# Kernel tuning notes

Measured on AMD Instinct MI355X. Metric: run time of the kernel, lower is better.

Reference implementation:

```python
import jax, jax.numpy as jnp
import numpy as np

DEGREE = 3
N_BASIS = 16


def _clamped_knots(n_basis, degree):
    # Clamped uniform knot vector on [0, 1]: degree+1 repeated knots at each end.
    n_interior = n_basis - degree - 1
    interior = np.linspace(0.0, 1.0, n_interior + 2)[1:-1]
    knots = np.concatenate([np.zeros(degree + 1), interior, np.ones(degree + 1)])
    return jnp.asarray(knots, dtype=jnp.float32)


def bspline_basis(x, degree=DEGREE, n_basis=N_BASIS):
    # Cox-de Boor recursion, vectorized over all leading dims of x.
    # x: (...,) in [0,1] -> (..., n_basis)
    t = _clamped_knots(n_basis, degree)
    n_knots = n_basis + degree + 1
    xe = jnp.clip(x, 0.0, 1.0 - 1e-6)[..., None]
    B = ((xe >= t[:-1]) & (xe < t[1:])).astype(x.dtype)  # (..., n_knots-1)
    for p in range(1, degree + 1):
        dl = t[p:n_knots - 1] - t[:n_knots - 1 - p]
        dr = t[p + 1:n_knots] - t[1:n_knots - p]
        left = jnp.where(dl > 0, (xe - t[:n_knots - 1 - p]) / jnp.where(dl > 0, dl, 1.0), 0.0)
        right = jnp.where(dr > 0, (t[p + 1:n_knots] - xe) / jnp.where(dr > 0, dr, 1.0), 0.0)
        B = left * B[..., :-1] + right * B[..., 1:]
    return B  # (..., n_basis)


def _kl(cm, lv):
    # KL(N(cm, exp(lv)) || N(0, 1)) summed over all edges/coeffs (prior_scale = 1).
    var = jnp.exp(lv)
    return 0.5 * jnp.sum(var + cm * cm - 1.0 - lv)


def _layer(x, cm, lv):
    # x: (B, in); cm, lv: (out, in, n_basis)
    basis = bspline_basis(x)  # (B, in, n_basis)
    out = jnp.einsum('bik,oik->bo', basis, cm)  # fused per-edge weighted sum
    return out, _kl(cm, lv)


def setup_inputs() -> dict:
    key = jax.random.key(0)
    ks = jax.random.split(key, 4)
    B = 8192
    sizes = [256, 512, 512, 256]
    nb = N_BASIS
    inp = {"x": jax.random.uniform(ks[0], (B, sizes[0]), dtype=jnp.float32)}
    for i in range(3):
        inp[f"cm{i}"] = 0.1 * jax.random.normal(ks[1 + i], (sizes[i + 1], sizes[i], nb), dtype=jnp.float32)
        inp[f"lv{i}"] = -2.0 * jnp.ones((sizes[i + 1], sizes[i], nb), dtype=jnp.float32)
    return inp


def reference(x, cm0, lv0, cm1, lv1, cm2, lv2):
    out = x
    kl = jnp.zeros((), x.dtype)
    for cm, lv in ((cm0, lv0), (cm1, lv1), (cm2, lv2)):
        out, k = _layer(out, cm, lv)
        kl = kl + k
    return out, kl
```

## Files before the change

### kernel.cpp

```cpp
#include <hip/hip_runtime.h>
#include <hip/hip_bf16.h>


typedef __attribute__((ext_vector_type(8))) _Float16 f16x8;
typedef __attribute__((ext_vector_type(4))) float float4v;
typedef unsigned short ushort_t;

__device__ __forceinline__ ushort_t f2h(float f) {
  _Float16 h = (_Float16)f;
  return *(ushort_t*)&h;
}
__device__ __forceinline__ float h2f(ushort_t u) {
  return (float)*(_Float16*)&u;
}

__device__ __forceinline__ void bspline_w4(float x, int& k0, float w[4]) {
  const float XMAX = 1.0f - 1e-6f;
  float xe = fminf(fmaxf(x, 0.0f), XMAX);
  int cell = (int)(xe * 13.0f);
  cell = cell > 12 ? 12 : cell;
  k0 = cell;
  int j = cell + 3;
  const float s = 1.0f / 13.0f;
  int cjm2 = max(j - 5, 0);
  int cjm1 = max(j - 4, 0);
  int cj   = j - 3;
  int cj1  = j - 2;
  int cj2  = min(j - 1, 13);
  int cj3  = min(j, 13);
  float tjm1 = cjm1 * s, tj = cj * s;
  float tjm2 = cjm2 * s;
  float tj1 = cj1 * s, tj2 = cj2 * s, tj3 = cj3 * s;
  float left1 = xe - tj, left2 = xe - tjm1, left3 = xe - tjm2;
  float right1 = tj1 - xe, right2 = tj2 - xe, right3 = tj3 - xe;
#define INV3(d) ((d) == 1 ? 13.0f : ((d) == 2 ? 6.5f : (13.0f / 3.0f)))
  float i10 = INV3(cj1 - cj);
  float i20 = INV3(cj1 - cjm1), i21 = INV3(cj2 - cj);
  float i30 = INV3(cj1 - cjm2), i31 = INV3(cj2 - cjm1), i32 = INV3(cj3 - cj);
#undef INV3
  float temp = i10;
  float N0 = right1 * temp;
  float N1 = left1 * temp;
  temp = N0 * i20;
  N0 = right1 * temp;
  float saved = left2 * temp;
  temp = N1 * i21;
  N1 = saved + right2 * temp;
  float N2 = left1 * temp;
  temp = N0 * i30;
  N0 = right1 * temp;
  saved = left3 * temp;
  temp = N1 * i31;
  N1 = saved + right2 * temp;
  saved = left2 * temp;
  temp = N2 * i32;
  N2 = saved + right3 * temp;
  float N3 = left1 * temp;
  w[0] = N0; w[1] = N1; w[2] = N2; w[3] = N3;
}

template <bool SPLIT_A>
__global__ __launch_bounds__(256, 2) void kan_layer(
    const float* __restrict__ act, const ushort_t* __restrict__ Bsw,
    float* __restrict__ outp, int IN, int OUT) {
  const int K = IN * 16;
  const int KC = K >> 3;
  __shared__ ushort_t Ah[128 * 72];
  __shared__ ushort_t Al[SPLIT_A ? 128 * 72 : 1];

  const int tid = threadIdx.x;
  const int lane = tid & 63;
  const int wv = tid >> 6;
  const int wm = wv >> 1, wn = wv & 1;
  const int quad = lane >> 4, l15 = lane & 15;
  const int b0 = blockIdx.x * 128;
  const int n0 = blockIdx.y * 128;
  const int tbase = (n0 >> 4) + wn * 4;

  float4v acc[4][4];
#pragma unroll
  for (int a = 0; a < 4; a++)
#pragma unroll
    for (int b = 0; b < 4; b++) acc[a][b] = (float4v)0.0f;

  const int gm = tid >> 1;
  const int gip = (tid & 1) * 2;

  const int nsteps = K / 64;
  const int chunk = nsteps / gridDim.z;
  const int kbeg = blockIdx.z * chunk;
  const int kend = kbeg + chunk;
  for (int kstep = kbeg; kstep < kend; ++kstep) {
    const int i0 = kstep * 4;

    const float2 xv = *(const float2*)&act[(size_t)(b0 + gm) * IN + i0 + gip];
    f16x8 bfrag[2][4];
#pragma unroll
    for (int ks = 0; ks < 2; ++ks)
#pragma unroll
      for (int nt = 0; nt < 4; ++nt) {
        size_t eoff = (((size_t)(tbase + nt)) * KC + kstep * 8 + ks * 4) * 128
                      + lane * 8;
        bfrag[ks][nt] = *(const f16x8*)&Bsw[eoff];
      }

    int k0a, k0b; float wa[4], wb[4];
    bspline_w4(xv.x, k0a, wa);
    bspline_w4(xv.y, k0b, wb);

    __syncthreads();

    {
      uint4 z; z.x = z.y = z.z = z.w = 0u;
      ushort_t* arow_h = &Ah[gm * 72 + gip * 16];
      ((uint4*)arow_h)[0] = z; ((uint4*)arow_h)[1] = z;
      ((uint4*)arow_h)[2] = z; ((uint4*)arow_h)[3] = z;
#pragma unroll
      for (int t = 0; t < 4; ++t) {
        arow_h[k0a + t] = f2h(wa[t]);
        arow_h[16 + k0b + t] = f2h(wb[t]);
      }
      if (SPLIT_A) {
        ushort_t* arow_l = &Al[gm * 72 + gip * 16];
        ((uint4*)arow_l)[0] = z; ((uint4*)arow_l)[1] = z;
        ((uint4*)arow_l)[2] = z; ((uint4*)arow_l)[3] = z;
#pragma unroll
        for (int t = 0; t < 4; ++t) {
          arow_l[k0a + t] = f2h(wa[t] - h2f(f2h(wa[t])));
          arow_l[16 + k0b + t] = f2h(wb[t] - h2f(f2h(wb[t])));
        }
      }
    }
    __syncthreads();

#pragma unroll
    for (int ks = 0; ks < 2; ++ks) {
      f16x8 ah[4], al[4];
#pragma unroll
      for (int mt = 0; mt < 4; ++mt) {
        int off = (wm * 64 + mt * 16 + l15) * 72 + ks * 32 + quad * 8;
        ah[mt] = *(const f16x8*)&Ah[off];
        if (SPLIT_A) al[mt] = *(const f16x8*)&Al[off];
      }
#pragma unroll
      for (int mt = 0; mt < 4; ++mt)
#pragma unroll
        for (int nt = 0; nt < 4; ++nt) {
          if (SPLIT_A)
            acc[mt][nt] = __builtin_amdgcn_mfma_f32_16x16x32_f16(al[mt], bfrag[ks][nt], acc[mt][nt], 0, 0, 0);
          acc[mt][nt] = __builtin_amdgcn_mfma_f32_16x16x32_f16(ah[mt], bfrag[ks][nt], acc[mt][nt], 0, 0, 0);
        }
    }
  }

#pragma unroll
  for (int mt = 0; mt < 4; ++mt)
#pragma unroll
    for (int nt = 0; nt < 4; ++nt) {
      int col = n0 + wn * 64 + nt * 16 + l15;
#pragma unroll
      for (int r = 0; r < 4; ++r) {
        int row = b0 + wm * 64 + mt * 16 + quad * 4 + r;
        atomicAdd(&outp[(size_t)row * OUT + col], acc[mt][nt][r]);
      }
    }
}

__global__ __launch_bounds__(256) void kl_convert(
    const float* __restrict__ cm, const float* __restrict__ lv,
    ushort_t* __restrict__ bsw, int G ,
    long long ngroups, float* __restrict__ klout) {
  long long i = (long long)blockIdx.x * blockDim.x + threadIdx.x;
  const long long stride = (long long)gridDim.x * blockDim.x;
  float s = 0.0f;
  for (; i < ngroups; i += stride) {
    int o = (int)(i / G);
    int kc = (int)(i - (long long)o * G);
    const float* cp = &cm[i * 8];
    const float* lp = &lv[i * 8];
    unsigned pk[4];
#pragma unroll
    for (int t = 0; t < 4; ++t) {
      float c0 = cp[2 * t], c1 = cp[2 * t + 1];
      float l0 = lp[2 * t], l1 = lp[2 * t + 1];
      pk[t] = (unsigned)f2h(c0) | ((unsigned)f2h(c1) << 16);
      s += 0.5f * (__expf(l0) + c0 * c0 - 1.0f - l0);
      s += 0.5f * (__expf(l1) + c1 * c1 - 1.0f - l1);
    }
    uint4 v; v.x = pk[0]; v.y = pk[1]; v.z = pk[2]; v.w = pk[3];
    size_t doff = (((size_t)(o >> 4) * G + kc) * 16 + (o & 15)) * 8;
    *(uint4*)&bsw[doff] = v;
  }
#pragma unroll
  for (int off = 32; off > 0; off >>= 1) s += __shfl_down(s, off, 64);
  __shared__ float red[4];
  int wv = threadIdx.x >> 6;
  if ((threadIdx.x & 63) == 0) red[wv] = s;
  __syncthreads();
  if (threadIdx.x == 0)
    atomicAdd(klout, red[0] + red[1] + red[2] + red[3]);
}

extern "C" void kernel_launch(void* const* d_in, const int* in_sizes, int n_in,
                              void* d_out, int out_size, void* d_ws, size_t ws_size,
                              hipStream_t stream) {
  const float* x   = (const float*)d_in[0];
  const float* cm0 = (const float*)d_in[1];
  const float* lv0 = (const float*)d_in[2];
  const float* cm1 = (const float*)d_in[3];
  const float* lv1 = (const float*)d_in[4];
  const float* cm2 = (const float*)d_in[5];
  const float* lv2 = (const float*)d_in[6];

  float* out = (float*)d_out;
  float* klp = out + (size_t)8192 * 256;

  char* ws = (char*)d_ws;
  float*    act1 = (float*)(ws);
  float*    act2 = (float*)(ws + ((size_t)16 << 20));
  ushort_t* b0sw = (ushort_t*)(ws + ((size_t)32 << 20));
  ushort_t* b1sw = (ushort_t*)(ws + ((size_t)36 << 20));
  ushort_t* b2sw = (ushort_t*)(ws + ((size_t)44 << 20));

  hipMemsetAsync(ws, 0, (size_t)32 << 20, stream);
  hipMemsetAsync(d_out, 0, (size_t)out_size * sizeof(float), stream);

  kl_convert<<<2048, 256, 0, stream>>>(cm0, lv0, b0sw, 256 * 2, 512LL * 256 * 2, klp);
  kl_convert<<<2048, 256, 0, stream>>>(cm1, lv1, b1sw, 512 * 2, 512LL * 512 * 2, klp);
  kl_convert<<<2048, 256, 0, stream>>>(cm2, lv2, b2sw, 512 * 2, 256LL * 512 * 2, klp);

  kan_layer<true ><<<dim3(64, 4, 4), 256, 0, stream>>>(x,    b0sw, act1, 256, 512);
  kan_layer<false><<<dim3(64, 4, 4), 256, 0, stream>>>(act1, b1sw, act2, 512, 512);
  kan_layer<false><<<dim3(64, 2, 8), 256, 0, stream>>>(act2, b2sw, out,  512, 256);
}
```

Measured before the change: 486.9 us.

## Per-wave private A tiles with swizzled LDS and register double-buffered B loads

Each wave now computes its own 64-row basis tile into a private, XOR-swizzled LDS region, built as full 16-byte packed stores, which removes both block-wide __syncthreads per k-step. B fragments and the next activations are prefetched one step ahead into a second register buffer. The cost is duplicated B-spline evaluation, since both wn waves compute the same rows, plus more LDS and higher register pressure, which could reduce occupancy under launch_bounds(256,2).

```diff
diff --git a/kernel.cpp b/kernel.cpp
--- a/kernel.cpp
+++ b/kernel.cpp
@@ -28,8 +28,7 @@
   int cj1  = j - 2;
   int cj2  = min(j - 1, 13);
   int cj3  = min(j, 13);
-  float tjm1 = cjm1 * s, tj = cj * s;
-  float tjm2 = cjm2 * s;
+  float tjm2 = cjm2 * s, tjm1 = cjm1 * s, tj = cj * s;
   float tj1 = cj1 * s, tj2 = cj2 * s, tj3 = cj3 * s;
   float left1 = xe - tj, left2 = xe - tjm1, left3 = xe - tjm2;
   float right1 = tj1 - xe, right2 = tj2 - xe, right3 = tj3 - xe;
@@ -59,14 +58,39 @@
   w[0] = N0; w[1] = N1; w[2] = N2; w[3] = N3;
 }
 
+__device__ __forceinline__ void compose16(const float w[4], int k0, unsigned u[8]) {
+  unsigned h0 = f2h(w[0]), h1 = f2h(w[1]), h2 = f2h(w[2]), h3 = f2h(w[3]);
+  int e = k0 >> 1;
+  bool odd = (k0 & 1) != 0;
+  unsigned a = odd ? (h0 << 16) : (h0 | (h1 << 16));
+  unsigned b = odd ? (h1 | (h2 << 16)) : (h2 | (h3 << 16));
+  unsigned c = odd ? (unsigned)h3 : 0u;
+#pragma unroll
+  for (int j = 0; j < 8; ++j)
+    u[j] = (j == e) ? a : (j == e + 1) ? b : (j == e + 2) ? c : 0u;
+}
+
+__device__ __forceinline__ void load_bfrags(const ushort_t* __restrict__ Bsw,
+                                            int tbase, int KC, int k, int lane,
+                                            f16x8 bf[2][4]) {
+#pragma unroll
+  for (int ks = 0; ks < 2; ++ks)
+#pragma unroll
+    for (int nt = 0; nt < 4; ++nt) {
+      size_t eoff = (((size_t)(tbase + nt)) * KC + (size_t)k * 8 + ks * 4) * 128
+                    + lane * 8;
+      bf[ks][nt] = *(const f16x8*)&Bsw[eoff];
+    }
+}
+
 template <bool SPLIT_A>
 __global__ __launch_bounds__(256, 2) void kan_layer(
     const float* __restrict__ act, const ushort_t* __restrict__ Bsw,
     float* __restrict__ outp, int IN, int OUT) {
   const int K = IN * 16;
   const int KC = K >> 3;
-  __shared__ ushort_t Ah[128 * 72];
-  __shared__ ushort_t Al[SPLIT_A ? 128 * 72 : 1];
+  __shared__ ushort_t Ah[4 * 64 * 64];
+  __shared__ ushort_t Al[SPLIT_A ? 4 * 64 * 64 : 1];
 
   const int tid = threadIdx.x;
   const int lane = tid & 63;
@@ -76,81 +100,75 @@
   const int b0 = blockIdx.x * 128;
   const int n0 = blockIdx.y * 128;
   const int tbase = (n0 >> 4) + wn * 4;
+  ushort_t* Awh = &Ah[wv * 4096];
+  ushort_t* Awl = SPLIT_A ? &Al[wv * 4096] : nullptr;
+  const int grow = b0 + wm * 64 + lane;
+  const int sw = (lane & 7);
 
   float4v acc[4][4];
 #pragma unroll
   for (int a = 0; a < 4; a++)
 #pragma unroll
     for (int b = 0; b < 4; b++) acc[a][b] = (float4v)0.0f;
-
-  const int gm = tid >> 1;
-  const int gip = (tid & 1) * 2;
 
   const int nsteps = K / 64;
   const int chunk = nsteps / gridDim.z;
   const int kbeg = blockIdx.z * chunk;
   const int kend = kbeg + chunk;
-  for (int kstep = kbeg; kstep < kend; ++kstep) {
-    const int i0 = kstep * 4;
-
-    const float2 xv = *(const float2*)&act[(size_t)(b0 + gm) * IN + i0 + gip];
-    f16x8 bfrag[2][4];
-#pragma unroll
-    for (int ks = 0; ks < 2; ++ks)
-#pragma unroll
-      for (int nt = 0; nt < 4; ++nt) {
-        size_t eoff = (((size_t)(tbase + nt)) * KC + kstep * 8 + ks * 4) * 128
-                      + lane * 8;
-        bfrag[ks][nt] = *(const f16x8*)&Bsw[eoff];
+
+  f16x8 bf[2][2][4];
+  float4 xv = *(const float4*)&act[(size_t)grow * IN + kbeg * 4];
+  load_bfrags(Bsw, tbase, KC, kbeg, lane, bf[0]);
+  int cur = 0;
+
+  for (int k = kbeg; k < kend; ++k) {
+    float4 xn = xv;
+    if (k + 1 < kend) {
+      xn = *(const float4*)&act[(size_t)grow * IN + (k + 1) * 4];
+      load_bfrags(Bsw, tbase, KC, k + 1, lane, bf[cur ^ 1]);
+    }
+
+#pragma unroll
+    for (int f = 0; f < 4; ++f) {
+      float xf = (f == 0) ? xv.x : (f == 1) ? xv.y : (f == 2) ? xv.z : xv.w;
+      int k0; float w[4];
+      bspline_w4(xf, k0, w);
+      unsigned u[8];
+      compose16(w, k0, u);
+      int s0 = ((2 * f) ^ sw) * 8;
+      int s1 = ((2 * f + 1) ^ sw) * 8;
+      *(uint4*)&Awh[lane * 64 + s0] = make_uint4(u[0], u[1], u[2], u[3]);
+      *(uint4*)&Awh[lane * 64 + s1] = make_uint4(u[4], u[5], u[6], u[7]);
+      if (SPLIT_A) {
+        float wl[4];
+#pragma unroll
+        for (int t = 0; t < 4; ++t) wl[t] = w[t] - h2f(f2h(w[t]));
+        compose16(wl, k0, u);
+        *(uint4*)&Awl[lane * 64 + s0] = make_uint4(u[0], u[1], u[2], u[3]);
+        *(uint4*)&Awl[lane * 64 + s1] = make_uint4(u[4], u[5], u[6], u[7]);
       }
-
-    int k0a, k0b; float wa[4], wb[4];
-    bspline_w4(xv.x, k0a, wa);
-    bspline_w4(xv.y, k0b, wb);
-
-    __syncthreads();
-
-    {
-      uint4 z; z.x = z.y = z.z = z.w = 0u;
-      ushort_t* arow_h = &Ah[gm * 72 + gip * 16];
-      ((uint4*)arow_h)[0] = z; ((uint4*)arow_h)[1] = z;
-      ((uint4*)arow_h)[2] = z; ((uint4*)arow_h)[3] = z;
-#pragma unroll
-      for (int t = 0; t < 4; ++t) {
-        arow_h[k0a + t] = f2h(wa[t]);
-        arow_h[16 + k0b + t] = f2h(wb[t]);
-      }
-      if (SPLIT_A) {
-        ushort_t* arow_l = &Al[gm * 72 + gip * 16];
-        ((uint4*)arow_l)[0] = z; ((uint4*)arow_l)[1] = z;
-        ((uint4*)arow_l)[2] = z; ((uint4*)arow_l)[3] = z;
-#pragma unroll
-        for (int t = 0; t < 4; ++t) {
-          arow_l[k0a + t] = f2h(wa[t] - h2f(f2h(wa[t])));
-          arow_l[16 + k0b + t] = f2h(wb[t] - h2f(f2h(wb[t])));
-        }
-      }
-    }
-    __syncthreads();
+    }
 
 #pragma unroll
     for (int ks = 0; ks < 2; ++ks) {
       f16x8 ah[4], al[4];
 #pragma unroll
       for (int mt = 0; mt < 4; ++mt) {
-        int off = (wm * 64 + mt * 16 + l15) * 72 + ks * 32 + quad * 8;
-        ah[mt] = *(const f16x8*)&Ah[off];
-        if (SPLIT_A) al[mt] = *(const f16x8*)&Al[off];
+        int off = (mt * 16 + l15) * 64 + (((ks * 4 + quad) ^ (l15 & 7)) * 8);
+        ah[mt] = *(const f16x8*)&Awh[off];
+        if (SPLIT_A) al[mt] = *(const f16x8*)&Awl[off];
       }
 #pragma unroll
       for (int mt = 0; mt < 4; ++mt)
 #pragma unroll
         for (int nt = 0; nt < 4; ++nt) {
           if (SPLIT_A)
-            acc[mt][nt] = __builtin_amdgcn_mfma_f32_16x16x32_f16(al[mt], bfrag[ks][nt], acc[mt][nt], 0, 0, 0);
-          acc[mt][nt] = __builtin_amdgcn_mfma_f32_16x16x32_f16(ah[mt], bfrag[ks][nt], acc[mt][nt], 0, 0, 0);
+            acc[mt][nt] = __builtin_amdgcn_mfma_f32_16x16x32_f16(al[mt], bf[cur][ks][nt], acc[mt][nt], 0, 0, 0);
+          acc[mt][nt] = __builtin_amdgcn_mfma_f32_16x16x32_f16(ah[mt], bf[cur][ks][nt], acc[mt][nt], 0, 0, 0);
         }
     }
+    xv = xn;
+    cur ^= 1;
   }
 
 #pragma unroll
@@ -194,8 +212,8 @@
 #pragma unroll
   for (int off = 32; off > 0; off >>= 1) s += __shfl_down(s, off, 64);
   __shared__ float red[4];
-  int wv = threadIdx.x >> 6;
-  if ((threadIdx.x & 63) == 0) red[wv] = s;
+  int wvi = threadIdx.x >> 6;
+  if ((threadIdx.x & 63) == 0) red[wvi] = s;
   __syncthreads();
   if (threadIdx.x == 0)
     atomicAdd(klout, red[0] + red[1] + red[2] + red[3]);
```

New measurement: 971.9 us. +99.6%, slower.
